# Optimization experiments

Measured on AMD Instinct MI355X. Metric: run time of the kernel, lower is better.

Reference implementation:

```python
import jax, jax.numpy as jnp
import numpy as np

N_HEADS = 8
D_EMBED = 512
D_HEAD = D_EMBED // N_HEADS


def setup_inputs() -> dict:
    key = jax.random.key(0)
    ks = jax.random.split(key, 5)
    x = jax.random.normal(ks[0], (1, 4096, D_EMBED), dtype=jnp.float32)
    # in_proj: Linear(d, 3d); out_proj: Linear(d, d). Stored as [in, out] for x @ W.
    scale_in = 1.0 / np.sqrt(D_EMBED)
    W_in = jax.random.uniform(ks[1], (D_EMBED, 3 * D_EMBED), jnp.float32, -scale_in, scale_in)
    b_in = jax.random.uniform(ks[2], (3 * D_EMBED,), jnp.float32, -scale_in, scale_in)
    W_out = jax.random.uniform(ks[3], (D_EMBED, D_EMBED), jnp.float32, -scale_in, scale_in)
    b_out = jax.random.uniform(ks[4], (D_EMBED,), jnp.float32, -scale_in, scale_in)
    return {"x": x, "W_in": W_in, "b_in": b_in, "W_out": W_out, "b_out": b_out,
            "causal_mask": 1}


def reference(x, W_in, b_in, W_out, b_out, causal_mask):
    B, S, D = x.shape
    qkv = x @ W_in + b_in                      # [B, S, 3D]
    q, k, v = jnp.split(qkv, 3, axis=-1)
    # [B, S, D] -> [B, H, S, d_head]
    def split_heads(t):
        return t.reshape(B, S, N_HEADS, D_HEAD).transpose(0, 2, 1, 3)
    q, k, v = split_heads(q), split_heads(k), split_heads(v)
    weight = jnp.einsum("bhqd,bhkd->bhqk", q, k)  # [B, H, S, S]
    if causal_mask:
        mask = jnp.triu(jnp.ones((S, S), dtype=bool), k=1)
        weight = jnp.where(mask, -jnp.inf, weight)
    weight = weight / jnp.sqrt(jnp.float32(D_HEAD)).astype(weight.dtype)
    weight = jax.nn.softmax(weight, axis=-1)
    out = jnp.einsum("bhqk,bhkd->bhqd", weight, v)  # [B, H, S, d_head]
    out = out.transpose(0, 2, 1, 3).reshape(B, S, D)
    return out @ W_out + b_out
```

## Files before the change

### kernel.cpp

```cpp
#include <hip/hip_runtime.h>
#include <math.h>

#define SEQ 4096
#define DM 512
#define NH 8
#define DH 64
#define TQK (3 * DM)

typedef __attribute__((ext_vector_type(8))) short bf16x8;
typedef __attribute__((ext_vector_type(4))) float floatx4;
typedef unsigned short ushort_t;

__device__ __forceinline__ floatx4 mfma16(bf16x8 a, bf16x8 b, floatx4 c) {
    return __builtin_amdgcn_mfma_f32_16x16x32_bf16(a, b, c, 0, 0, 0);
}

__device__ __forceinline__ unsigned int pk2(float a, float b) {
    unsigned int ua = __float_as_uint(a); ua = (ua + 0x7FFFu + ((ua >> 16) & 1u)) >> 16;
    unsigned int ub = __float_as_uint(b); ub = (ub + 0x7FFFu + ((ub >> 16) & 1u)) >> 16;
    return ua | (ub << 16);
}
__device__ __forceinline__ unsigned short f2bf(float x) {
    unsigned int u = __float_as_uint(x);
    return (unsigned short)((u + 0x7FFFu + ((u >> 16) & 1u)) >> 16);
}
__device__ __forceinline__ float bflo(unsigned int u) { return __uint_as_float(u << 16); }
__device__ __forceinline__ float bfhi(unsigned int u) { return __uint_as_float(u & 0xFFFF0000u); }

__device__ __forceinline__ void gload_lds16(const void* g, void* l) {
    __builtin_amdgcn_global_load_lds(
        (const __attribute__((address_space(1))) unsigned int*)g,
        (__attribute__((address_space(3))) unsigned int*)l, 16, 0, 0);
}

#define DPPMAX(x, ctrl) \
    (x) = fmaxf((x), __int_as_float(__builtin_amdgcn_update_dpp(0, __float_as_int(x), (ctrl), 0xF, 0xF, true)))
__device__ __forceinline__ float row_max16(float x) {
    DPPMAX(x, 0xB1);
    DPPMAX(x, 0x4E);
    DPPMAX(x, 0x141);
    DPPMAX(x, 0x140);
    return x;
}

__global__ __launch_bounds__(256) void f2bf_vec(const float* __restrict__ in,
                                                ushort_t* __restrict__ out) {
    const int i = blockIdx.x * 256 + threadIdx.x;
    const float4* p = (const float4*)in + (size_t)i * 2;
    float4 f0 = p[0], f1 = p[1];
    ((uint4*)out)[i] = make_uint4(pk2(f0.x, f0.y), pk2(f0.z, f0.w),
                                  pk2(f1.x, f1.y), pk2(f1.z, f1.w));
}

__global__ __launch_bounds__(256) void wt_bf16(const float* __restrict__ W,
                                               ushort_t* __restrict__ WT,
                                               int K, int N, int scale_below) {
    __shared__ float T[64][65];
    const int tid = threadIdx.x;
    const int k0 = blockIdx.y * 64, n0 = blockIdx.x * 64;
    {
        const int r = tid >> 2, g = tid & 3;
        const float* src = W + (size_t)(k0 + r) * N + n0 + g * 16;
#pragma unroll
        for (int i = 0; i < 4; i++) {
            float4 f = ((const float4*)src)[i];
            T[g * 16 + i * 4 + 0][r] = f.x;
            T[g * 16 + i * 4 + 1][r] = f.y;
            T[g * 16 + i * 4 + 2][r] = f.z;
            T[g * 16 + i * 4 + 3][r] = f.w;
        }
    }
    __syncthreads();
    const int nr = tid >> 2, g2 = tid & 3;
    const float sc = (n0 + nr < scale_below) ? 0.125f : 1.0f;
    unsigned int pk[8];
#pragma unroll
    for (int j = 0; j < 8; j++)
        pk[j] = pk2(T[nr][g2 * 16 + 2 * j] * sc, T[nr][g2 * 16 + 2 * j + 1] * sc);
    ushort_t* dst = WT + (size_t)(n0 + nr) * K + k0 + g2 * 16;
    ((uint4*)dst)[0] = make_uint4(pk[0], pk[1], pk[2], pk[3]);
    ((uint4*)dst)[1] = make_uint4(pk[4], pk[5], pk[6], pk[7]);
}

template <bool OUT_BF16>
__global__ __launch_bounds__(256) void gemm_mfma(const ushort_t* __restrict__ A,
                                                 const ushort_t* __restrict__ BT,
                                                 const float* __restrict__ bias,
                                                 void* __restrict__ Cv,
                                                 ushort_t* __restrict__ vt_out,
                                                 int M, int N, int K, int scale_below) {
    __shared__ __align__(16) ushort_t As[128 * 64];
    __shared__ __align__(16) ushort_t Bs[64 * 64];
    const int tid  = threadIdx.x;
    const int lane = tid & 63;
    const int w    = tid >> 6;
    const int quad = lane >> 4;
    const int ln   = lane & 15;
    const int row0 = blockIdx.y * 128;
    const int col0 = blockIdx.x * 64;
    const int wm = w >> 1, wn = w & 1;

    const int srow = lane >> 3;
    const int js   = (lane & 7) ^ srow;

    floatx4 acc[4][2];
#pragma unroll
    for (int i = 0; i < 4; i++)
#pragma unroll
        for (int j = 0; j < 2; j++) acc[i][j] = (floatx4){0.f, 0.f, 0.f, 0.f};

    for (int k0 = 0; k0 < K; k0 += 64) {
        __syncthreads();
#pragma unroll
        for (int i = 0; i < 4; i++) {
            const int c = w * 4 + i;
            gload_lds16(A + (size_t)(row0 + c * 8 + srow) * K + k0 + js * 8, &As[c * 512]);
        }
#pragma unroll
        for (int i = 0; i < 2; i++) {
            const int c = w * 2 + i;
            gload_lds16(BT + (size_t)(col0 + c * 8 + srow) * K + k0 + js * 8, &Bs[c * 512]);
        }
        __syncthreads();

#pragma unroll
        for (int s = 0; s < 2; s++) {
            bf16x8 af[4], bfr[2];
#pragma unroll
            for (int i = 0; i < 4; i++) {
                const int lm = wm * 64 + i * 16 + ln;
                af[i] = *(const bf16x8*)&As[lm * 64 + ((s * 4 + quad) ^ (ln & 7)) * 8];
            }
#pragma unroll
            for (int j = 0; j < 2; j++) {
                const int lnn = wn * 32 + j * 16 + ln;
                bfr[j] = *(const bf16x8*)&Bs[lnn * 64 + ((s * 4 + quad) ^ (ln & 7)) * 8];
            }
#pragma unroll
            for (int i = 0; i < 4; i++)
#pragma unroll
                for (int j = 0; j < 2; j++)
                    acc[i][j] = mfma16(af[i], bfr[j], acc[i][j]);
        }
    }

    if (vt_out && col0 >= 2 * DM) {
#pragma unroll
        for (int j = 0; j < 2; j++) {
            const int n = col0 + wn * 32 + j * 16 + ln;
            const float bv = bias[n];
#pragma unroll
            for (int i = 0; i < 4; i++) {
                const int mb = row0 + wm * 64 + i * 16 + quad * 4;
                uint2 pkd;
                pkd.x = pk2(acc[i][j][0] + bv, acc[i][j][1] + bv);
                pkd.y = pk2(acc[i][j][2] + bv, acc[i][j][3] + bv);
                *(uint2*)&vt_out[(size_t)(n - 2 * DM) * SEQ + mb] = pkd;
            }
        }
        return;
    }

#pragma unroll
    for (int j = 0; j < 2; j++) {
        const int n = col0 + wn * 32 + j * 16 + ln;
        const float bv = bias[n] * ((n < scale_below) ? 0.125f : 1.0f);
#pragma unroll
        for (int i = 0; i < 4; i++) {
            const int mb = row0 + wm * 64 + i * 16 + quad * 4;
#pragma unroll
            for (int r = 0; r < 4; r++) {
                const float v = acc[i][j][r] + bv;
                if (OUT_BF16) ((ushort_t*)Cv)[(size_t)(mb + r) * N + n] = f2bf(v);
                else          ((float*)Cv)[(size_t)(mb + r) * N + n] = v;
            }
        }
    }
}

__global__ __launch_bounds__(256) void attn_split(const ushort_t* __restrict__ qkv_b,
                                                  const ushort_t* __restrict__ vt,
                                                  ushort_t* __restrict__ po,
                                                  float2* __restrict__ pml) {
    __shared__ __align__(16) ushort_t Ks[64 * 64];
    __shared__ __align__(16) ushort_t Vs[64 * 64];
    __shared__ __align__(16) ushort_t Ps[64 * 72];

    const int tid  = threadIdx.x;
    const int lane = tid & 63;
    const int w    = tid >> 6;
    const int quad = lane >> 4;
    const int ln   = lane & 15;
    const int h    = blockIdx.y;

    const int e = 159 - (int)blockIdx.x;
    int qt, nc, c;
    if (e < 16)      { qt = e;                      nc = 1; c = 0; }
    else if (e < 48) { qt = 16 + ((e - 16) >> 1);   nc = 2; c = (e - 16) & 1; }
    else if (e < 96) { int u = e - 48; int q = u / 3; qt = 32 + q; nc = 3; c = u - 3 * q; }
    else             { int u = e - 96; qt = 48 + (u >> 2); nc = 4; c = u & 3; }
    const int T   = qt + 1;
    const int jt0 = (c * T) / nc;
    const int jt1 = ((c + 1) * T) / nc;
    const int q0  = qt * 64;

    const ushort_t* qrow = qkv_b + (size_t)(q0 + w * 16 + ln) * TQK + h * DH;
    const bf16x8 a0 = *(const bf16x8*)(qrow + quad * 8);
    const bf16x8 a1 = *(const bf16x8*)(qrow + quad * 8 + 32);

    const short oneb = (short)0x3F80;
    const bf16x8 vone = {oneb, oneb, oneb, oneb, oneb, oneb, oneb, oneb};

    float m_r[4];
    floatx4 o[4], ol;
#pragma unroll
    for (int r = 0; r < 4; r++) m_r[r] = -INFINITY;
#pragma unroll
    for (int t = 0; t < 4; t++) o[t] = (floatx4){0.f, 0.f, 0.f, 0.f};
    ol = (floatx4){0.f, 0.f, 0.f, 0.f};

    const int srow = lane >> 3;
    const int js   = (lane & 7) ^ srow;

    for (int jt = jt0; jt < jt1; ++jt) {
        const int k0 = jt * 64;
        __syncthreads();
#pragma unroll
        for (int i = 0; i < 2; i++) {
            const int cg = w * 2 + i;
            gload_lds16(qkv_b + (size_t)(k0 + cg * 8 + srow) * TQK + DM + h * DH + js * 8,
                        &Ks[cg * 512]);
            gload_lds16(vt + (size_t)(h * DH + cg * 8 + srow) * SEQ + k0 + js * 8,
                        &Vs[cg * 512]);
        }
        __syncthreads();

        floatx4 sa[4];
#pragma unroll
        for (int t = 0; t < 4; t++) {
            const int n = t * 16 + ln;
            const bf16x8 b0 = *(const bf16x8*)&Ks[n * 64 + ((quad) ^ (ln & 7)) * 8];
            const bf16x8 b1 = *(const bf16x8*)&Ks[n * 64 + ((4 + quad) ^ (ln & 7)) * 8];
            floatx4 acc = {0.f, 0.f, 0.f, 0.f};
            acc = mfma16(a0, b0, acc);
            acc = mfma16(a1, b1, acc);
            sa[t] = acc;
        }

        if (jt == qt) {
#pragma unroll
            for (int t = 0; t < 4; t++) {
                const int cg = t * 16 + ln;
#pragma unroll
                for (int r = 0; r < 4; r++) {
                    const int rg = w * 16 + quad * 4 + r;
                    if (cg > rg) sa[t][r] = -INFINITY;
                }
            }
        }

#pragma unroll
        for (int r = 0; r < 4; r++) {
            float mx = fmaxf(fmaxf(sa[0][r], sa[1][r]), fmaxf(sa[2][r], sa[3][r]));
            mx = row_max16(mx);
            const float mn = fmaxf(m_r[r], mx);
            const float alpha = __expf(m_r[r] - mn);
            m_r[r] = mn;
#pragma unroll
            for (int t = 0; t < 4; t++) {
                const float p = __expf(sa[t][r] - mn);
                Ps[(w * 16 + quad * 4 + r) * 72 + t * 16 + ln] = f2bf(p);
            }
#pragma unroll
            for (int t = 0; t < 4; t++) o[t][r] *= alpha;
            ol[r] *= alpha;
        }

        __builtin_amdgcn_wave_barrier();

        const bf16x8 p0 = *(const bf16x8*)&Ps[(w * 16 + ln) * 72 + quad * 8];
        const bf16x8 p1 = *(const bf16x8*)&Ps[(w * 16 + ln) * 72 + quad * 8 + 32];
#pragma unroll
        for (int t = 0; t < 4; t++) {
            const int d = t * 16 + ln;
            const bf16x8 v0 = *(const bf16x8*)&Vs[d * 64 + ((quad) ^ (ln & 7)) * 8];
            const bf16x8 v1 = *(const bf16x8*)&Vs[d * 64 + ((4 + quad) ^ (ln & 7)) * 8];
            o[t] = mfma16(p0, v0, o[t]);
            o[t] = mfma16(p1, v1, o[t]);
        }
        ol = mfma16(p0, vone, ol);
        ol = mfma16(p1, vone, ol);
    }

    const size_t pbase  = (((size_t)h * 64 + qt) * 4 + c) * (64 * 64);
    const size_t mlbase = (((size_t)h * 64 + qt) * 4 + c) * 64;
#pragma unroll
    for (int t = 0; t < 4; t++)
#pragma unroll
        for (int r = 0; r < 4; r++)
            po[pbase + (size_t)(w * 16 + quad * 4 + r) * 64 + t * 16 + ln] = f2bf(o[t][r]);
    if (ln == 0) {
#pragma unroll
        for (int r = 0; r < 4; r++)
            pml[mlbase + w * 16 + quad * 4 + r] = make_float2(m_r[r], ol[r]);
    }
}

__global__ __launch_bounds__(256) void attn_combine(const ushort_t* __restrict__ po,
                                                    const float2* __restrict__ pml,
                                                    ushort_t* __restrict__ aob) {
    const int qt = blockIdx.x, h = blockIdx.y;
    const int nc = (qt >> 4) + 1;
    const int row = threadIdx.x >> 2, g = threadIdx.x & 3;
    const size_t base   = (((size_t)h * 64 + qt) * 4) * (64 * 64);
    const size_t mlbase = (((size_t)h * 64 + qt) * 4) * 64;

    float2 ml[4];
    float M = -INFINITY;
    for (int cidx = 0; cidx < nc; cidx++) {
        ml[cidx] = pml[mlbase + (size_t)cidx * 64 + row];
        M = fmaxf(M, ml[cidx].x);
    }
    float L = 0.f;
    float acc[16];
#pragma unroll
    for (int j = 0; j < 16; j++) acc[j] = 0.f;

    for (int cidx = 0; cidx < nc; cidx++) {
        const float wgt = __expf(ml[cidx].x - M);
        L += wgt * ml[cidx].y;
        const ushort_t* p = po + base + (size_t)cidx * 4096 + (size_t)row * 64 + g * 16;
        uint4 u0 = ((const uint4*)p)[0];
        uint4 u1 = ((const uint4*)p)[1];
        const unsigned int uu[8] = {u0.x, u0.y, u0.z, u0.w, u1.x, u1.y, u1.z, u1.w};
#pragma unroll
        for (int j = 0; j < 8; j++) {
            acc[2 * j]     += wgt * bflo(uu[j]);
            acc[2 * j + 1] += wgt * bfhi(uu[j]);
        }
    }
    const float inv = 1.0f / L;
    unsigned int pk[8];
#pragma unroll
    for (int j = 0; j < 8; j++)
        pk[j] = pk2(acc[2 * j] * inv, acc[2 * j + 1] * inv);
    ushort_t* dst = aob + (size_t)(qt * 64 + row) * DM + h * DH + g * 16;
    ((uint4*)dst)[0] = make_uint4(pk[0], pk[1], pk[2], pk[3]);
    ((uint4*)dst)[1] = make_uint4(pk[4], pk[5], pk[6], pk[7]);
}

extern "C" void kernel_launch(void* const* d_in, const int* in_sizes, int n_in,
                              void* d_out, int out_size, void* d_ws, size_t ws_size,
                              hipStream_t stream) {
    const float* x     = (const float*)d_in[0];
    const float* W_in  = (const float*)d_in[1];
    const float* b_in  = (const float*)d_in[2];
    const float* W_out = (const float*)d_in[3];
    const float* b_out = (const float*)d_in[4];
    float* out = (float*)d_out;

    char* ws = (char*)d_ws;
    ushort_t* xb    = (ushort_t*)ws;
    ushort_t* wti   = (ushort_t*)(ws + (4u  << 20));
    ushort_t* wto   = (ushort_t*)(ws + (6u  << 20));
    ushort_t* qkv_b = (ushort_t*)(ws + (7u  << 20));
    ushort_t* vtb   = (ushort_t*)(ws + (19u << 20));
    ushort_t* aob   = (ushort_t*)(ws + (23u << 20));
    ushort_t* po    = (ushort_t*)(ws + (27u << 20));
    float2*   pml   = (float2*)  (ws + (43u << 20));

    f2bf_vec<<<SEQ * DM / 8 / 256, 256, 0, stream>>>(x, xb);
    wt_bf16<<<dim3(TQK / 64, DM / 64), 256, 0, stream>>>(W_in, wti, DM, TQK, DM);
    wt_bf16<<<dim3(DM / 64, DM / 64), 256, 0, stream>>>(W_out, wto, DM, DM, 0);

    gemm_mfma<true><<<dim3(TQK / 64, SEQ / 128), 256, 0, stream>>>(
        xb, wti, b_in, qkv_b, vtb, SEQ, TQK, DM, DM);

    attn_split<<<dim3(160, NH), 256, 0, stream>>>(qkv_b, vtb, po, pml);

    attn_combine<<<dim3(SEQ / 64, NH), 256, 0, stream>>>(po, pml, aob);

    gemm_mfma<false><<<dim3(DM / 64, SEQ / 128), 256, 0, stream>>>(
        aob, wto, b_out, out, nullptr, SEQ, DM, DM, 0);
}
```

Measured before the change: 188.2 us.

## Fuse prep kernels, double-buffer GEMM and attention, finer KV split, exp2 softmax

Merges the three conversion and transpose kernels into one launch. Widens the GEMM tile to 128x128 with double-buffered LDS prefetch, and double-buffers the K/V tiles in attention. Reworks the attention work split so query tiles are divided into up to 8 KV chunks across 288 blocks, and folds log2(e) into the Q scale so softmax can use exp2. Uses one max per wave instead of per row, truncates P to bf16 instead of rounding, and skips the rescale when the max is unchanged. The costs are more LDS per block, fewer GEMM blocks for the output projection, and small precision changes.

```diff
diff --git a/kernel.cpp b/kernel.cpp
--- a/kernel.cpp
+++ b/kernel.cpp
@@ -6,6 +6,7 @@
 #define NH 8
 #define DH 64
 #define TQK (3 * DM)
+#define QSCALE 0.18033688011112042f
 
 typedef __attribute__((ext_vector_type(8))) short bf16x8;
 typedef __attribute__((ext_vector_type(4))) float floatx4;
@@ -14,6 +15,7 @@
 __device__ __forceinline__ floatx4 mfma16(bf16x8 a, bf16x8 b, floatx4 c) {
     return __builtin_amdgcn_mfma_f32_16x16x32_bf16(a, b, c, 0, 0, 0);
 }
+__device__ __forceinline__ float ex2(float x) { return __builtin_amdgcn_exp2f(x); }
 
 __device__ __forceinline__ unsigned int pk2(float a, float b) {
     unsigned int ua = __float_as_uint(a); ua = (ua + 0x7FFFu + ((ua >> 16) & 1u)) >> 16;
@@ -43,21 +45,27 @@
     return x;
 }
 
-__global__ __launch_bounds__(256) void f2bf_vec(const float* __restrict__ in,
-                                                ushort_t* __restrict__ out) {
-    const int i = blockIdx.x * 256 + threadIdx.x;
-    const float4* p = (const float4*)in + (size_t)i * 2;
-    float4 f0 = p[0], f1 = p[1];
-    ((uint4*)out)[i] = make_uint4(pk2(f0.x, f0.y), pk2(f0.z, f0.w),
-                                  pk2(f1.x, f1.y), pk2(f1.z, f1.w));
-}
-
-__global__ __launch_bounds__(256) void wt_bf16(const float* __restrict__ W,
-                                               ushort_t* __restrict__ WT,
-                                               int K, int N, int scale_below) {
+__global__ __launch_bounds__(256) void prep(const float* __restrict__ x,
+                                            const float* __restrict__ W_in,
+                                            const float* __restrict__ W_out,
+                                            ushort_t* __restrict__ xb,
+                                            ushort_t* __restrict__ wti,
+                                            ushort_t* __restrict__ wto) {
     __shared__ float T[64][65];
-    const int tid = threadIdx.x;
-    const int k0 = blockIdx.y * 64, n0 = blockIdx.x * 64;
+    const int bid = blockIdx.x, tid = threadIdx.x;
+    if (bid < 1024) {
+        const int i = bid * 256 + tid;
+        const float4* p = (const float4*)x + (size_t)i * 2;
+        float4 f0 = p[0], f1 = p[1];
+        ((uint4*)xb)[i] = make_uint4(pk2(f0.x, f0.y), pk2(f0.z, f0.w),
+                                     pk2(f1.x, f1.y), pk2(f1.z, f1.w));
+        return;
+    }
+    const float* W; ushort_t* WT; int N, K, n0, k0; bool qscale;
+    if (bid < 1216) { int id = bid - 1024; W = W_in;  WT = wti; N = TQK; K = DM;
+                      n0 = (id % 24) * 64; k0 = (id / 24) * 64; qscale = true; }
+    else            { int id = bid - 1216; W = W_out; WT = wto; N = DM;  K = DM;
+                      n0 = (id % 8) * 64;  k0 = (id / 8) * 64;  qscale = false; }
     {
         const int r = tid >> 2, g = tid & 3;
         const float* src = W + (size_t)(k0 + r) * N + n0 + g * 16;
@@ -72,7 +80,7 @@
     }
     __syncthreads();
     const int nr = tid >> 2, g2 = tid & 3;
-    const float sc = (n0 + nr < scale_below) ? 0.125f : 1.0f;
+    const float sc = (qscale && (n0 + nr < DM)) ? QSCALE : 1.0f;
     unsigned int pk[8];
 #pragma unroll
     for (int j = 0; j < 8; j++)
@@ -83,71 +91,74 @@
 }
 
 template <bool OUT_BF16>
-__global__ __launch_bounds__(256) void gemm_mfma(const ushort_t* __restrict__ A,
-                                                 const ushort_t* __restrict__ BT,
-                                                 const float* __restrict__ bias,
-                                                 void* __restrict__ Cv,
-                                                 ushort_t* __restrict__ vt_out,
-                                                 int M, int N, int K, int scale_below) {
-    __shared__ __align__(16) ushort_t As[128 * 64];
-    __shared__ __align__(16) ushort_t Bs[64 * 64];
+__global__ __launch_bounds__(256) void gemm128(const ushort_t* __restrict__ A,
+                                               const ushort_t* __restrict__ BT,
+                                               const float* __restrict__ bias,
+                                               void* __restrict__ Cv,
+                                               ushort_t* __restrict__ vt_out,
+                                               int N, int K, int scale_q) {
+    __shared__ __align__(16) ushort_t As[2][128 * 64];
+    __shared__ __align__(16) ushort_t Bs[2][128 * 64];
     const int tid  = threadIdx.x;
     const int lane = tid & 63;
     const int w    = tid >> 6;
     const int quad = lane >> 4;
     const int ln   = lane & 15;
     const int row0 = blockIdx.y * 128;
-    const int col0 = blockIdx.x * 64;
+    const int col0 = blockIdx.x * 128;
     const int wm = w >> 1, wn = w & 1;
 
     const int srow = lane >> 3;
     const int js   = (lane & 7) ^ srow;
 
-    floatx4 acc[4][2];
+    floatx4 acc[4][4];
 #pragma unroll
     for (int i = 0; i < 4; i++)
 #pragma unroll
-        for (int j = 0; j < 2; j++) acc[i][j] = (floatx4){0.f, 0.f, 0.f, 0.f};
-
-    for (int k0 = 0; k0 < K; k0 += 64) {
+        for (int j = 0; j < 4; j++) acc[i][j] = (floatx4){0.f, 0.f, 0.f, 0.f};
+
+    const int nsteps = K >> 6;
+#pragma unroll
+    for (int i = 0; i < 4; i++) {
+        const int c = w * 4 + i;
+        gload_lds16(A  + (size_t)(row0 + c * 8 + srow) * K + js * 8, &As[0][c * 512]);
+        gload_lds16(BT + (size_t)(col0 + c * 8 + srow) * K + js * 8, &Bs[0][c * 512]);
+    }
+
+    for (int kt = 0; kt < nsteps; kt++) {
+        const int cur = kt & 1;
         __syncthreads();
-#pragma unroll
-        for (int i = 0; i < 4; i++) {
-            const int c = w * 4 + i;
-            gload_lds16(A + (size_t)(row0 + c * 8 + srow) * K + k0 + js * 8, &As[c * 512]);
-        }
-#pragma unroll
-        for (int i = 0; i < 2; i++) {
-            const int c = w * 2 + i;
-            gload_lds16(BT + (size_t)(col0 + c * 8 + srow) * K + k0 + js * 8, &Bs[c * 512]);
-        }
-        __syncthreads();
-
+        if (kt + 1 < nsteps) {
+            const int k0n = (kt + 1) << 6;
+#pragma unroll
+            for (int i = 0; i < 4; i++) {
+                const int c = w * 4 + i;
+                gload_lds16(A  + (size_t)(row0 + c * 8 + srow) * K + k0n + js * 8, &As[cur ^ 1][c * 512]);
+                gload_lds16(BT + (size_t)(col0 + c * 8 + srow) * K + k0n + js * 8, &Bs[cur ^ 1][c * 512]);
+            }
+        }
 #pragma unroll
         for (int s = 0; s < 2; s++) {
-            bf16x8 af[4], bfr[2];
+            bf16x8 af[4], bfr[4];
 #pragma unroll
             for (int i = 0; i < 4; i++) {
                 const int lm = wm * 64 + i * 16 + ln;
-                af[i] = *(const bf16x8*)&As[lm * 64 + ((s * 4 + quad) ^ (ln & 7)) * 8];
-            }
-#pragma unroll
-            for (int j = 0; j < 2; j++) {
-                const int lnn = wn * 32 + j * 16 + ln;
-                bfr[j] = *(const bf16x8*)&Bs[lnn * 64 + ((s * 4 + quad) ^ (ln & 7)) * 8];
+                af[i] = *(const bf16x8*)&As[cur][lm * 64 + ((s * 4 + quad) ^ (ln & 7)) * 8];
+                const int lnn = wn * 64 + i * 16 + ln;
+                bfr[i] = *(const bf16x8*)&Bs[cur][lnn * 64 + ((s * 4 + quad) ^ (ln & 7)) * 8];
             }
 #pragma unroll
             for (int i = 0; i < 4; i++)
 #pragma unroll
-                for (int j = 0; j < 2; j++)
+                for (int j = 0; j < 4; j++)
                     acc[i][j] = mfma16(af[i], bfr[j], acc[i][j]);
         }
     }
 
     if (vt_out && col0 >= 2 * DM) {
 #pragma unroll
-        for (int j = 0; j < 2; j++) {
-            const int n = col0 + wn * 32 + j * 16 + ln;
+        for (int j = 0; j < 4; j++) {
+            const int n = col0 + wn * 64 + j * 16 + ln;
             const float bv = bias[n];
 #pragma unroll
             for (int i = 0; i < 4; i++) {
@@ -162,9 +173,9 @@
     }
 
 #pragma unroll
-    for (int j = 0; j < 2; j++) {
-        const int n = col0 + wn * 32 + j * 16 + ln;
-        const float bv = bias[n] * ((n < scale_below) ? 0.125f : 1.0f);
+    for (int j = 0; j < 4; j++) {
+        const int n = col0 + wn * 64 + j * 16 + ln;
+        const float bv = bias[n] * ((scale_q && n < DM) ? QSCALE : 1.0f);
 #pragma unroll
         for (int i = 0; i < 4; i++) {
             const int mb = row0 + wm * 64 + i * 16 + quad * 4;
@@ -182,8 +193,8 @@
                                                   const ushort_t* __restrict__ vt,
                                                   ushort_t* __restrict__ po,
                                                   float2* __restrict__ pml) {
-    __shared__ __align__(16) ushort_t Ks[64 * 64];
-    __shared__ __align__(16) ushort_t Vs[64 * 64];
+    __shared__ __align__(16) ushort_t Ks[2][64 * 64];
+    __shared__ __align__(16) ushort_t Vs[2][64 * 64];
     __shared__ __align__(16) ushort_t Ps[64 * 72];
 
     const int tid  = threadIdx.x;
@@ -193,12 +204,13 @@
     const int ln   = lane & 15;
     const int h    = blockIdx.y;
 
-    const int e = 159 - (int)blockIdx.x;
-    int qt, nc, c;
-    if (e < 16)      { qt = e;                      nc = 1; c = 0; }
-    else if (e < 48) { qt = 16 + ((e - 16) >> 1);   nc = 2; c = (e - 16) & 1; }
-    else if (e < 96) { int u = e - 48; int q = u / 3; qt = 32 + q; nc = 3; c = u - 3 * q; }
-    else             { int u = e - 96; qt = 48 + (u >> 2); nc = 4; c = u & 3; }
+    const int e = 287 - (int)blockIdx.x;
+    int k = 1;
+    while (e >= 4 * k * (k + 1)) k++;
+    const int off = e - 4 * k * (k - 1);
+    const int qt  = 8 * (k - 1) + off / k;
+    const int c   = off % k;
+    const int nc  = k;
     const int T   = qt + 1;
     const int jt0 = (c * T) / nc;
     const int jt1 = ((c + 1) * T) / nc;
@@ -211,10 +223,8 @@
     const short oneb = (short)0x3F80;
     const bf16x8 vone = {oneb, oneb, oneb, oneb, oneb, oneb, oneb, oneb};
 
-    float m_r[4];
+    float m_q = -INFINITY;
     floatx4 o[4], ol;
-#pragma unroll
-    for (int r = 0; r < 4; r++) m_r[r] = -INFINITY;
 #pragma unroll
     for (int t = 0; t < 4; t++) o[t] = (floatx4){0.f, 0.f, 0.f, 0.f};
     ol = (floatx4){0.f, 0.f, 0.f, 0.f};
@@ -222,25 +232,39 @@
     const int srow = lane >> 3;
     const int js   = (lane & 7) ^ srow;
 
-    for (int jt = jt0; jt < jt1; ++jt) {
-        const int k0 = jt * 64;
-        __syncthreads();
+    {
+        const int k0 = jt0 * 64;
 #pragma unroll
         for (int i = 0; i < 2; i++) {
             const int cg = w * 2 + i;
             gload_lds16(qkv_b + (size_t)(k0 + cg * 8 + srow) * TQK + DM + h * DH + js * 8,
-                        &Ks[cg * 512]);
+                        &Ks[0][cg * 512]);
             gload_lds16(vt + (size_t)(h * DH + cg * 8 + srow) * SEQ + k0 + js * 8,
-                        &Vs[cg * 512]);
-        }
+                        &Vs[0][cg * 512]);
+        }
+    }
+
+    for (int jt = jt0; jt < jt1; ++jt) {
+        const int cur = (jt - jt0) & 1;
         __syncthreads();
+        if (jt + 1 < jt1) {
+            const int k0n = (jt + 1) * 64;
+#pragma unroll
+            for (int i = 0; i < 2; i++) {
+                const int cg = w * 2 + i;
+                gload_lds16(qkv_b + (size_t)(k0n + cg * 8 + srow) * TQK + DM + h * DH + js * 8,
+                            &Ks[cur ^ 1][cg * 512]);
+                gload_lds16(vt + (size_t)(h * DH + cg * 8 + srow) * SEQ + k0n + js * 8,
+                            &Vs[cur ^ 1][cg * 512]);
+            }
+        }
 
         floatx4 sa[4];
 #pragma unroll
         for (int t = 0; t < 4; t++) {
             const int n = t * 16 + ln;
-            const bf16x8 b0 = *(const bf16x8*)&Ks[n * 64 + ((quad) ^ (ln & 7)) * 8];
-            const bf16x8 b1 = *(const bf16x8*)&Ks[n * 64 + ((4 + quad) ^ (ln & 7)) * 8];
+            const bf16x8 b0 = *(const bf16x8*)&Ks[cur][n * 64 + ((quad) ^ (ln & 7)) * 8];
+            const bf16x8 b1 = *(const bf16x8*)&Ks[cur][n * 64 + ((4 + quad) ^ (ln & 7)) * 8];
             floatx4 acc = {0.f, 0.f, 0.f, 0.f};
             acc = mfma16(a0, b0, acc);
             acc = mfma16(a1, b1, acc);
@@ -250,30 +274,39 @@
         if (jt == qt) {
 #pragma unroll
             for (int t = 0; t < 4; t++) {
-                const int cg = t * 16 + ln;
+                const int cg2 = t * 16 + ln;
 #pragma unroll
                 for (int r = 0; r < 4; r++) {
                     const int rg = w * 16 + quad * 4 + r;
-                    if (cg > rg) sa[t][r] = -INFINITY;
+                    if (cg2 > rg) sa[t][r] = -INFINITY;
                 }
             }
         }
 
-#pragma unroll
-        for (int r = 0; r < 4; r++) {
-            float mx = fmaxf(fmaxf(sa[0][r], sa[1][r]), fmaxf(sa[2][r], sa[3][r]));
-            mx = row_max16(mx);
-            const float mn = fmaxf(m_r[r], mx);
-            const float alpha = __expf(m_r[r] - mn);
-            m_r[r] = mn;
-#pragma unroll
-            for (int t = 0; t < 4; t++) {
-                const float p = __expf(sa[t][r] - mn);
-                Ps[(w * 16 + quad * 4 + r) * 72 + t * 16 + ln] = f2bf(p);
-            }
-#pragma unroll
-            for (int t = 0; t < 4; t++) o[t][r] *= alpha;
-            ol[r] *= alpha;
+        float mx = sa[0][0];
+#pragma unroll
+        for (int t = 0; t < 4; t++)
+#pragma unroll
+            for (int r = 0; r < 4; r++) mx = fmaxf(mx, sa[t][r]);
+        mx = row_max16(mx);
+        const float mn = fmaxf(m_q, mx);
+        const float alpha = ex2(m_q - mn);
+        m_q = mn;
+#pragma unroll
+        for (int t = 0; t < 4; t++)
+#pragma unroll
+            for (int r = 0; r < 4; r++) {
+                const float p = ex2(sa[t][r] - mn);
+                Ps[(w * 16 + quad * 4 + r) * 72 + t * 16 + ln] =
+                    (ushort_t)(__float_as_uint(p) >> 16);
+            }
+        if (alpha < 1.0f) {
+#pragma unroll
+            for (int t = 0; t < 4; t++)
+#pragma unroll
+                for (int r = 0; r < 4; r++) o[t][r] *= alpha;
+#pragma unroll
+            for (int r = 0; r < 4; r++) ol[r] *= alpha;
         }
 
         __builtin_amdgcn_wave_barrier();
@@ -283,8 +316,8 @@
 #pragma unroll
         for (int t = 0; t < 4; t++) {
             const int d = t * 16 + ln;
-            const bf16x8 v0 = *(const bf16x8*)&Vs[d * 64 + ((quad) ^ (ln & 7)) * 8];
-            const bf16x8 v1 = *(const bf16x8*)&Vs[d * 64 + ((4 + quad) ^ (ln & 7)) * 8];
+            const bf16x8 v0 = *(const bf16x8*)&Vs[cur][d * 64 + ((quad) ^ (ln & 7)) * 8];
+            const bf16x8 v1 = *(const bf16x8*)&Vs[cur][d * 64 + ((4 + quad) ^ (ln & 7)) * 8];
             o[t] = mfma16(p0, v0, o[t]);
             o[t] = mfma16(p1, v1, o[t]);
         }
@@ -292,8 +325,8 @@
         ol = mfma16(p1, vone, ol);
     }
 
-    const size_t pbase  = (((size_t)h * 64 + qt) * 4 + c) * (64 * 64);
-    const size_t mlbase = (((size_t)h * 64 + qt) * 4 + c) * 64;
+    const size_t pbase  = ((size_t)h * 288 + e) * 4096;
+    const size_t mlbase = ((size_t)h * 288 + e) * 64;
 #pragma unroll
     for (int t = 0; t < 4; t++)
 #pragma unroll
@@ -302,7 +335,7 @@
     if (ln == 0) {
 #pragma unroll
         for (int r = 0; r < 4; r++)
-            pml[mlbase + w * 16 + quad * 4 + r] = make_float2(m_r[r], ol[r]);
+            pml[mlbase + w * 16 + quad * 4 + r] = make_float2(m_q, ol[r]);
     }
 }
 
@@ -310,15 +343,15 @@
                                                     const float2* __restrict__ pml,
                                                     ushort_t* __restrict__ aob) {
     const int qt = blockIdx.x, h = blockIdx.y;
-    const int nc = (qt >> 4) + 1;
+    const int k = (qt >> 3) + 1;
+    const int sbase = 4 * k * (k - 1) + (qt & 7) * k;
+    const int nc = k;
     const int row = threadIdx.x >> 2, g = threadIdx.x & 3;
-    const size_t base   = (((size_t)h * 64 + qt) * 4) * (64 * 64);
-    const size_t mlbase = (((size_t)h * 64 + qt) * 4) * 64;
-
-    float2 ml[4];
+
+    float2 ml[8];
     float M = -INFINITY;
     for (int cidx = 0; cidx < nc; cidx++) {
-        ml[cidx] = pml[mlbase + (size_t)cidx * 64 + row];
+        ml[cidx] = pml[((size_t)h * 288 + sbase + cidx) * 64 + row];
         M = fmaxf(M, ml[cidx].x);
     }
     float L = 0.f;
@@ -327,9 +360,9 @@
     for (int j = 0; j < 16; j++) acc[j] = 0.f;
 
     for (int cidx = 0; cidx < nc; cidx++) {
-        const float wgt = __expf(ml[cidx].x - M);
+        const float wgt = ex2(ml[cidx].x - M);
         L += wgt * ml[cidx].y;
-        const ushort_t* p = po + base + (size_t)cidx * 4096 + (size_t)row * 64 + g * 16;
+        const ushort_t* p = po + ((size_t)h * 288 + sbase + cidx) * 4096 + (size_t)row * 64 + g * 16;
         uint4 u0 = ((const uint4*)p)[0];
         uint4 u1 = ((const uint4*)p)[1];
         const unsigned int uu[8] = {u0.x, u0.y, u0.z, u0.w, u1.x, u1.y, u1.z, u1.w};
@@ -367,19 +400,17 @@
     ushort_t* vtb   = (ushort_t*)(ws + (19u << 20));
     ushort_t* aob   = (ushort_t*)(ws + (23u << 20));
     ushort_t* po    = (ushort_t*)(ws + (27u << 20));
-    float2*   pml   = (float2*)  (ws + (43u << 20));
-
-    f2bf_vec<<<SEQ * DM / 8 / 256, 256, 0, stream>>>(x, xb);
-    wt_bf16<<<dim3(TQK / 64, DM / 64), 256, 0, stream>>>(W_in, wti, DM, TQK, DM);
-    wt_bf16<<<dim3(DM / 64, DM / 64), 256, 0, stream>>>(W_out, wto, DM, DM, 0);
-
-    gemm_mfma<true><<<dim3(TQK / 64, SEQ / 128), 256, 0, stream>>>(
-        xb, wti, b_in, qkv_b, vtb, SEQ, TQK, DM, DM);
-
-    attn_split<<<dim3(160, NH), 256, 0, stream>>>(qkv_b, vtb, po, pml);
+    float2*   pml   = (float2*)  (ws + (46u << 20));
+
+    prep<<<1280, 256, 0, stream>>>(x, W_in, W_out, xb, wti, wto);
+
+    gemm128<true><<<dim3(TQK / 128, SEQ / 128), 256, 0, stream>>>(
+        xb, wti, b_in, qkv_b, vtb, TQK, DM, 1);
+
+    attn_split<<<dim3(288, NH), 256, 0, stream>>>(qkv_b, vtb, po, pml);
 
     attn_combine<<<dim3(SEQ / 64, NH), 256, 0, stream>>>(po, pml, aob);
 
-    gemm_mfma<false><<<dim3(DM / 64, SEQ / 128), 256, 0, stream>>>(
-        aob, wto, b_out, out, nullptr, SEQ, DM, DM, 0);
-}
+    gemm128<false><<<dim3(DM / 128, SEQ / 128), 256, 0, stream>>>(
+        aob, wto, b_out, out, nullptr, DM, DM, 0);
+}
```

After: 173.7 us. 7.7% less time.
